# Performance work log

Hardware: AMD Instinct MI355X
Metric: run time of the kernel (lower is better)

## Reference

```python
import jax, jax.numpy as jnp
import numpy as np

B, N1, N2, D = 8, 2048, 2048, 512

def setup_inputs() -> dict:
    key = jax.random.key(0)
    k1, k2, k3, k4 = jax.random.split(key, 4)
    input1 = jax.random.normal(k1, (B, N1, D), dtype=jnp.float32)
    input2 = jax.random.normal(k2, (B, N2, D), dtype=jnp.float32)
    # nn.Linear(D, D): weight [D, D] (out, in), bias [D]
    W_w = jax.random.normal(k3, (D, D), dtype=jnp.float32) * (1.0 / np.sqrt(D))
    W_b = jax.random.normal(k4, (D,), dtype=jnp.float32) * 0.01
    return {"input1": input1, "input2": input2, "W_w": W_w, "W_b": W_b}

def reference(input1, input2, W_w, W_b):
    # q = W(input1): [B, N1, D]
    q = jnp.einsum('bnd,od->bno', input1, W_w) + W_b
    # unscaled scores softmax over last dim (keys N2)
    attn = jax.nn.softmax(jnp.einsum('bnd,bmd->bnm', q, input2), axis=-1)  # [B, N1, N2]
    output1 = jnp.einsum('bnm,bmd->bnd', attn, input2)   # [B, N1, D]
    output2 = jnp.einsum('bnm,bnd->bmd', attn, input1)   # attn^T @ input1 -> [B, N2, D]
    return (output1, output2)
```

## Files before the change

### kernel.cpp

```cpp
#include <hip/hip_runtime.h>


typedef _Float16 f16x8 __attribute__((ext_vector_type(8)));
typedef float floatx4 __attribute__((ext_vector_type(4)));
typedef __attribute__((address_space(1))) const void* gptr_t;
typedef __attribute__((address_space(3))) void* lptr_t;

union F8 { f16x8 v; _Float16 h[8]; unsigned short u[8]; unsigned w[4]; };

__device__ __forceinline__ void gld16(const void* g, void* l) {
    __builtin_amdgcn_global_load_lds((gptr_t)g, (lptr_t)l, 16, 0, 0);
}
__device__ __forceinline__ floatx4 mfma16(f16x8 a, f16x8 b, floatx4 c) {
    return __builtin_amdgcn_mfma_f32_16x16x32_f16(a, b, c, 0, 0, 0);
}

template <int ROWS>
__device__ __forceinline__ void stage64(const _Float16* g, int ldg,
                                        _Float16* lds, int tid) {
#pragma unroll
    for (int c = 0; c < (ROWS * 8) / 256; ++c) {
        const int q = c * 256 + tid;
        const int row = q >> 3;
        const int oct = (q & 7) ^ (row & 7);
        gld16(g + (size_t)row * ldg + oct * 8, lds + q * 8);
    }
}
__device__ __forceinline__ f16x8 ldfrag64(const _Float16* lds, int row, int j) {
    return *(const f16x8*)&lds[row * 64 + ((j ^ (row & 7)) << 3)];
}

template <int ROWS>
__device__ __forceinline__ void stage128(const _Float16* g, int ldg,
                                         _Float16* lds, int tid) {
#pragma unroll
    for (int c = 0; c < (ROWS * 16) / 256; ++c) {
        const int q = c * 256 + tid;
        const int row = q >> 4;
        const int oct = (q & 15) ^ (row & 15);
        gld16(g + (size_t)row * ldg + oct * 8, lds + q * 8);
    }
}
__device__ __forceinline__ f16x8 ldfrag128(const _Float16* lds, int row, int j) {
    return *(const f16x8*)&lds[row * 128 + ((j ^ (row & 15)) << 3)];
}

__global__ __launch_bounds__(256) void k_prep2(
    const float* __restrict__ in1, const float* __restrict__ in2,
    _Float16* __restrict__ x16, _Float16* __restrict__ xt,
    _Float16* __restrict__ k16, _Float16* __restrict__ vt)
{
    const int z = blockIdx.z;
    const int b = z & 7;
    const float* src = (z < 8 ? in1 : in2);
    _Float16* rowo = (z < 8 ? x16 : k16);
    _Float16* colo = (z < 8 ? xt : vt);
    const int d0 = blockIdx.x * 128, n0 = blockIdx.y * 32;
    const float* Sp = src + (size_t)b * 2048 * 512;
    _Float16* Rp = rowo + (size_t)b * 2048 * 512;
    _Float16* Cp = colo + (size_t)b * 512 * 2048;
    const int t = threadIdx.x, i = t & 63, jn = t >> 6;
    const int d = d0 + 2 * i, n = n0 + jn * 8;
    F8 w0, w1;
#pragma unroll
    for (int j = 0; j < 8; j++) {
        float2 g = *(const float2*)(Sp + (size_t)(n + j) * 512 + d);
        w0.h[j] = (_Float16)g.x; w1.h[j] = (_Float16)g.y;
        F8 r; r.h[0] = w0.h[j]; r.h[1] = w1.h[j];
        *(unsigned*)(Rp + (size_t)(n + j) * 512 + d) = r.w[0];
    }
    *(f16x8*)(Cp + (size_t)d * 2048 + n) = w0.v;
    *(f16x8*)(Cp + (size_t)(d + 1) * 2048 + n) = w1.v;
}

__global__ __launch_bounds__(256) void k_cvt(const float* __restrict__ src,
                                             _Float16* __restrict__ dst)
{
    const size_t i = ((size_t)blockIdx.x * 256 + threadIdx.x) * 8;
    float4 a = *(const float4*)(src + i);
    float4 b = *(const float4*)(src + i + 4);
    F8 w;
    w.h[0] = (_Float16)a.x; w.h[1] = (_Float16)a.y;
    w.h[2] = (_Float16)a.z; w.h[3] = (_Float16)a.w;
    w.h[4] = (_Float16)b.x; w.h[5] = (_Float16)b.y;
    w.h[6] = (_Float16)b.z; w.h[7] = (_Float16)b.w;
    *(f16x8*)(dst + i) = w.v;
}

__global__ __launch_bounds__(256, 4) void k_qgemm16(
    const _Float16* __restrict__ A, const _Float16* __restrict__ W,
    const float* __restrict__ bias, _Float16* __restrict__ q)
{
    __shared__ __align__(16) _Float16 As[128 * 64], Bs[128 * 64];
    const int tid = threadIdx.x;
    const int lane = tid & 63, wave = tid >> 6;
    const int wM = (wave >> 1) * 64, wN = (wave & 1) * 64;
    const int lrow = lane & 15, kq = lane >> 4;
    const int bi = blockIdx.x;
    const int r0 = (bi >> 2) * 128, c0 = (bi & 3) * 128;

    floatx4 acc[4][4];
#pragma unroll
    for (int i = 0; i < 4; i++)
#pragma unroll
        for (int j = 0; j < 4; j++) acc[i][j] = (floatx4){0.f, 0.f, 0.f, 0.f};

    for (int k0 = 0; k0 < 512; k0 += 64) {
        stage64<128>(A + (size_t)r0 * 512 + k0, 512, As, tid);
        stage64<128>(W + (size_t)c0 * 512 + k0, 512, Bs, tid);
        __syncthreads();
#pragma unroll
        for (int ks = 0; ks < 2; ks++) {
            f16x8 a[4], b[4];
#pragma unroll
            for (int i = 0; i < 4; i++) {
                a[i] = ldfrag64(As, wM + i * 16 + lrow, ks * 4 + kq);
                b[i] = ldfrag64(Bs, wN + i * 16 + lrow, ks * 4 + kq);
            }
#pragma unroll
            for (int mi = 0; mi < 4; mi++)
#pragma unroll
                for (int ni = 0; ni < 4; ni++)
                    acc[mi][ni] = mfma16(a[mi], b[ni], acc[mi][ni]);
        }
        __syncthreads();
    }
#pragma unroll
    for (int ni = 0; ni < 4; ni++) {
        const int col = c0 + wN + ni * 16 + lrow;
        const float bv = bias[col];
#pragma unroll
        for (int mi = 0; mi < 4; mi++) {
            const int row = r0 + wM + mi * 16 + kq * 4;
#pragma unroll
            for (int r = 0; r < 4; r++)
                q[(size_t)(row + r) * 512 + col] = (_Float16)(acc[mi][ni][r] + bv);
        }
    }
}

__global__ __launch_bounds__(256, 4) void k_scores16(
    const _Float16* __restrict__ q, const _Float16* __restrict__ k,
    _Float16* __restrict__ S)
{
    __shared__ __align__(16) _Float16 As[128 * 64], Bs[128 * 64];
    const int tid = threadIdx.x;
    const int lane = tid & 63, wave = tid >> 6;
    const int wM = (wave >> 1) * 64, wN = (wave & 1) * 64;
    const int lrow = lane & 15, kq = lane >> 4;
    const int bi = blockIdx.x;
    const int bz = bi & 7, t = bi >> 3;
    const int c0 = (t & 15) * 128, r0 = (t >> 4) * 128;
    const _Float16* qp = q + (size_t)bz * 2048 * 512;
    const _Float16* kp = k + (size_t)bz * 2048 * 512;
    _Float16* Sp = S + (size_t)bz * 2048 * 2048;

    floatx4 acc[4][4];
#pragma unroll
    for (int i = 0; i < 4; i++)
#pragma unroll
        for (int j = 0; j < 4; j++) acc[i][j] = (floatx4){0.f, 0.f, 0.f, 0.f};

    for (int k0 = 0; k0 < 512; k0 += 64) {
        stage64<128>(qp + (size_t)r0 * 512 + k0, 512, As, tid);
        stage64<128>(kp + (size_t)c0 * 512 + k0, 512, Bs, tid);
        __syncthreads();
#pragma unroll
        for (int ks = 0; ks < 2; ks++) {
            f16x8 a[4], b[4];
#pragma unroll
            for (int i = 0; i < 4; i++) {
                a[i] = ldfrag64(As, wM + i * 16 + lrow, ks * 4 + kq);
                b[i] = ldfrag64(Bs, wN + i * 16 + lrow, ks * 4 + kq);
            }
#pragma unroll
            for (int mi = 0; mi < 4; mi++)
#pragma unroll
                for (int ni = 0; ni < 4; ni++)
                    acc[mi][ni] = mfma16(a[mi], b[ni], acc[mi][ni]);
        }
        __syncthreads();
    }
#pragma unroll
    for (int mi = 0; mi < 4; mi++)
#pragma unroll
        for (int ni = 0; ni < 4; ni++) {
            const int row = r0 + wM + mi * 16 + kq * 4;
            const int col = c0 + wN + ni * 16 + lrow;
            _Float16* dst = Sp + (size_t)row * 2048 + col;
#pragma unroll
            for (int r = 0; r < 4; r++) dst[(size_t)r * 2048] = (_Float16)acc[mi][ni][r];
        }
}

__global__ __launch_bounds__(256) void k_softmax(const _Float16* __restrict__ S,
                                                 _Float16* __restrict__ P)
{
    const int row = blockIdx.x;
    const _Float16* s = S + (size_t)row * 2048;
    _Float16* p = P + (size_t)row * 2048;
    const int tid = threadIdx.x;
    const int lane = tid & 63, wave = tid >> 6;

    F8 raw;
    raw.v = *(const f16x8*)(s + tid * 8);
    float v[8];
#pragma unroll
    for (int i = 0; i < 8; i++) v[i] = (float)raw.h[i];
    float m = fmaxf(fmaxf(fmaxf(v[0], v[1]), fmaxf(v[2], v[3])),
                    fmaxf(fmaxf(v[4], v[5]), fmaxf(v[6], v[7])));
#pragma unroll
    for (int off = 32; off >= 1; off >>= 1) m = fmaxf(m, __shfl_down(m, off));
    __shared__ float rb[4];
    if (lane == 0) rb[wave] = m;
    __syncthreads();
    m = fmaxf(fmaxf(rb[0], rb[1]), fmaxf(rb[2], rb[3]));

    float e[8];
#pragma unroll
    for (int i = 0; i < 8; i++) e[i] = __expf(v[i] - m);
    float sum = ((e[0] + e[1]) + (e[2] + e[3])) + ((e[4] + e[5]) + (e[6] + e[7]));
#pragma unroll
    for (int off = 32; off >= 1; off >>= 1) sum += __shfl_down(sum, off);
    __syncthreads();
    if (lane == 0) rb[wave] = sum;
    __syncthreads();
    const float inv = 1.0f / (((rb[0] + rb[1]) + (rb[2] + rb[3])));

    F8 w;
#pragma unroll
    for (int i = 0; i < 8; i++) w.h[i] = (_Float16)(e[i] * inv);
    *(f16x8*)(p + tid * 8) = w.v;
}

#define ASTR 136
__global__ __launch_bounds__(256, 3) void k_out12(
    const _Float16* __restrict__ P, const _Float16* __restrict__ Vt,
    const _Float16* __restrict__ Xt, float* __restrict__ O1,
    float* __restrict__ O2)
{
    __shared__ __align__(16) _Float16 As[64 * ASTR];
    __shared__ __align__(16) _Float16 Bs[128 * 128];
    const int tid = threadIdx.x;
    const int lane = tid & 63, wave = tid >> 6;
    const int wM = (wave >> 1) * 32, wN = (wave & 1) * 64;
    const int lrow = lane & 15, kq = lane >> 4;
    const bool isO2 = blockIdx.x >= 1024;
    const int bi = blockIdx.x & 1023;
    const int bz = bi & 7, t = bi >> 3;
    const int c0 = (t & 3) * 128, r0 = (t >> 2) * 64;
    const _Float16* Pp = P + (size_t)bz * 2048 * 2048;
    const _Float16* Bp = (isO2 ? Xt : Vt) + (size_t)bz * 512 * 2048;
    float* Op = (isO2 ? O2 : O1) + (size_t)bz * 2048 * 512;

    floatx4 acc[2][4];
#pragma unroll
    for (int i = 0; i < 2; i++)
#pragma unroll
        for (int j = 0; j < 4; j++) acc[i][j] = (floatx4){0.f, 0.f, 0.f, 0.f};

    if (!isO2) {
        for (int k0 = 0; k0 < 2048; k0 += 128) {
            stage128<64>(Pp + (size_t)r0 * 2048 + k0, 2048, As, tid);
            stage128<128>(Bp + (size_t)c0 * 2048 + k0, 2048, Bs, tid);
            __syncthreads();
#pragma unroll
            for (int ks = 0; ks < 4; ks++) {
                f16x8 a[2], b[4];
#pragma unroll
                for (int i = 0; i < 2; i++)
                    a[i] = ldfrag128(As, wM + i * 16 + lrow, ks * 4 + kq);
#pragma unroll
                for (int i = 0; i < 4; i++)
                    b[i] = ldfrag128(Bs, wN + i * 16 + lrow, ks * 4 + kq);
#pragma unroll
                for (int mi = 0; mi < 2; mi++)
#pragma unroll
                    for (int ni = 0; ni < 4; ni++)
                        acc[mi][ni] = mfma16(a[mi], b[ni], acc[mi][ni]);
            }
            __syncthreads();
        }
    } else {
        const int mPair = (tid & 31) * 2;
        const int kOct0 = tid >> 5;
        for (int k0 = 0; k0 < 2048; k0 += 128) {
            stage128<128>(Bp + (size_t)c0 * 2048 + k0, 2048, Bs, tid);
#pragma unroll
            for (int kh = 0; kh < 2; kh++) {
                const int kOct = kOct0 + kh * 8;
                F8 w0, w1;
#pragma unroll
                for (int j = 0; j < 8; j++) {
                    const unsigned g = *(const unsigned*)(
                        Pp + (size_t)(k0 + kOct * 8 + j) * 2048 + r0 + mPair);
                    w0.u[j] = (unsigned short)(g & 0xffffu);
                    w1.u[j] = (unsigned short)(g >> 16);
                }
                *(f16x8*)&As[mPair * ASTR + kOct * 8] = w0.v;
                *(f16x8*)&As[(mPair + 1) * ASTR + kOct * 8] = w1.v;
            }
            __syncthreads();
#pragma unroll
            for (int ks = 0; ks < 4; ks++) {
                f16x8 a[2], b[4];
#pragma unroll
                for (int i = 0; i < 2; i++)
                    a[i] = *(const f16x8*)&As[(wM + i * 16 + lrow) * ASTR +
                                              (ks * 4 + kq) * 8];
#pragma unroll
                for (int i = 0; i < 4; i++)
                    b[i] = ldfrag128(Bs, wN + i * 16 + lrow, ks * 4 + kq);
#pragma unroll
                for (int mi = 0; mi < 2; mi++)
#pragma unroll
                    for (int ni = 0; ni < 4; ni++)
                        acc[mi][ni] = mfma16(a[mi], b[ni], acc[mi][ni]);
            }
            __syncthreads();
        }
    }
#pragma unroll
    for (int mi = 0; mi < 2; mi++)
#pragma unroll
        for (int ni = 0; ni < 4; ni++) {
            const int row = r0 + wM + mi * 16 + kq * 4;
            const int col = c0 + wN + ni * 16 + lrow;
            float* dst = Op + (size_t)row * 512 + col;
#pragma unroll
            for (int r = 0; r < 4; r++) dst[(size_t)r * 512] = acc[mi][ni][r];
        }
}

extern "C" void kernel_launch(void* const* d_in, const int* in_sizes, int n_in,
                              void* d_out, int out_size, void* d_ws, size_t ws_size,
                              hipStream_t stream)
{
    (void)in_sizes; (void)n_in; (void)out_size; (void)ws_size;
    const float* in1 = (const float*)d_in[0];
    const float* in2 = (const float*)d_in[1];
    const float* Ww  = (const float*)d_in[2];
    const float* Wb  = (const float*)d_in[3];
    float* out = (float*)d_out;

    char* ws = (char*)d_ws;
    _Float16* S   = (_Float16*)ws;
    _Float16* P   = (_Float16*)(ws + 67108864ull);
    _Float16* q16 = (_Float16*)(ws + 134217728ull);
    _Float16* x16 = (_Float16*)(ws + 150994944ull);
    _Float16* k16 = (_Float16*)(ws + 167772160ull);
    _Float16* vt  = (_Float16*)(ws + 184549376ull);
    _Float16* xt  = (_Float16*)(ws + 201326592ull);
    _Float16* w16 = (_Float16*)(ws + 218103808ull);

    k_prep2<<<dim3(4, 64, 16), 256, 0, stream>>>(in1, in2, x16, xt, k16, vt);
    k_cvt <<<128, 256, 0, stream>>>(Ww, w16);
    k_qgemm16<<<512, 256, 0, stream>>>(x16, w16, Wb, q16);
    k_scores16<<<2048, 256, 0, stream>>>(q16, k16, S);
    k_softmax<<<16384, 256, 0, stream>>>(S, P);
    k_out12<<<2048, 256, 0, stream>>>(P, vt, xt, out, out + 8388608);
}
```

Before: 307.7 us.

## Double-buffer output GEMMs, split out kernels, wave-per-row softmax, LDS-tiled transpose prep

The combined output kernel is split into separate O1 and O2 kernels. Both now double-buffer their LDS tiles, and O2 prefetches its transposed P loads into registers so global latency overlaps the MFMA work. Softmax now gives each wave one full row, using xor shuffles with no block barriers. The prep kernel transposes through an LDS tile so its global reads and writes are wide and coalesced. The cost is more LDS per block, which lowers occupancy for O2 (launch bound 2), plus an extra kernel launch.

```diff
diff --git a/kernel.cpp b/kernel.cpp
--- a/kernel.cpp
+++ b/kernel.cpp
@@ -2,11 +2,13 @@
 
 
 typedef _Float16 f16x8 __attribute__((ext_vector_type(8)));
+typedef _Float16 f16x4 __attribute__((ext_vector_type(4)));
 typedef float floatx4 __attribute__((ext_vector_type(4)));
 typedef __attribute__((address_space(1))) const void* gptr_t;
 typedef __attribute__((address_space(3))) void* lptr_t;
 
 union F8 { f16x8 v; _Float16 h[8]; unsigned short u[8]; unsigned w[4]; };
+union F4 { f16x4 v; _Float16 h[4]; unsigned u2[2]; };
 
 __device__ __forceinline__ void gld16(const void* g, void* l) {
     __builtin_amdgcn_global_load_lds((gptr_t)g, (lptr_t)l, 16, 0, 0);
@@ -45,32 +47,46 @@
     return *(const f16x8*)&lds[row * 128 + ((j ^ (row & 15)) << 3)];
 }
 
+#define TS 66
 __global__ __launch_bounds__(256) void k_prep2(
     const float* __restrict__ in1, const float* __restrict__ in2,
     _Float16* __restrict__ x16, _Float16* __restrict__ xt,
     _Float16* __restrict__ k16, _Float16* __restrict__ vt)
 {
+    __shared__ __align__(16) _Float16 T[64 * TS];
     const int z = blockIdx.z;
     const int b = z & 7;
     const float* src = (z < 8 ? in1 : in2);
     _Float16* rowo = (z < 8 ? x16 : k16);
     _Float16* colo = (z < 8 ? xt : vt);
-    const int d0 = blockIdx.x * 128, n0 = blockIdx.y * 32;
+    const int d0 = blockIdx.x * 64, n0 = blockIdx.y * 64;
     const float* Sp = src + (size_t)b * 2048 * 512;
     _Float16* Rp = rowo + (size_t)b * 2048 * 512;
     _Float16* Cp = colo + (size_t)b * 512 * 2048;
-    const int t = threadIdx.x, i = t & 63, jn = t >> 6;
-    const int d = d0 + 2 * i, n = n0 + jn * 8;
+    const int t = threadIdx.x;
+
+#pragma unroll
+    for (int c = 0; c < 4; c++) {
+        const int q = c * 256 + t, r = q >> 4, c4 = q & 15;
+        const float4 g = *(const float4*)(Sp + (size_t)(n0 + r) * 512 + d0 + c4 * 4);
+        F4 w;
+        w.h[0] = (_Float16)g.x; w.h[1] = (_Float16)g.y;
+        w.h[2] = (_Float16)g.z; w.h[3] = (_Float16)g.w;
+        *(f16x4*)(Rp + (size_t)(n0 + r) * 512 + d0 + c4 * 4) = w.v;
+        *(unsigned*)&T[r * TS + c4 * 4]     = w.u2[0];
+        *(unsigned*)&T[r * TS + c4 * 4 + 2] = w.u2[1];
+    }
+    __syncthreads();
+    const int c8 = t & 7, drp = (t >> 3) * 2;
     F8 w0, w1;
 #pragma unroll
-    for (int j = 0; j < 8; j++) {
-        float2 g = *(const float2*)(Sp + (size_t)(n + j) * 512 + d);
-        w0.h[j] = (_Float16)g.x; w1.h[j] = (_Float16)g.y;
-        F8 r; r.h[0] = w0.h[j]; r.h[1] = w1.h[j];
-        *(unsigned*)(Rp + (size_t)(n + j) * 512 + d) = r.w[0];
-    }
-    *(f16x8*)(Cp + (size_t)d * 2048 + n) = w0.v;
-    *(f16x8*)(Cp + (size_t)(d + 1) * 2048 + n) = w1.v;
+    for (int i = 0; i < 8; i++) {
+        const unsigned g = *(const unsigned*)&T[(c8 * 8 + i) * TS + drp];
+        w0.u[i] = (unsigned short)(g & 0xffffu);
+        w1.u[i] = (unsigned short)(g >> 16);
+    }
+    *(f16x8*)(Cp + (size_t)(d0 + drp) * 2048 + n0 + c8 * 8) = w0.v;
+    *(f16x8*)(Cp + (size_t)(d0 + drp + 1) * 2048 + n0 + c8 * 8) = w1.v;
 }
 
 __global__ __launch_bounds__(256) void k_cvt(const float* __restrict__ src,
@@ -196,62 +212,56 @@
 __global__ __launch_bounds__(256) void k_softmax(const _Float16* __restrict__ S,
                                                  _Float16* __restrict__ P)
 {
-    const int row = blockIdx.x;
+    const int wave = threadIdx.x >> 6, lane = threadIdx.x & 63;
+    const int row = blockIdx.x * 4 + wave;
     const _Float16* s = S + (size_t)row * 2048;
     _Float16* p = P + (size_t)row * 2048;
-    const int tid = threadIdx.x;
-    const int lane = tid & 63, wave = tid >> 6;
-
-    F8 raw;
-    raw.v = *(const f16x8*)(s + tid * 8);
-    float v[8];
-#pragma unroll
-    for (int i = 0; i < 8; i++) v[i] = (float)raw.h[i];
-    float m = fmaxf(fmaxf(fmaxf(v[0], v[1]), fmaxf(v[2], v[3])),
-                    fmaxf(fmaxf(v[4], v[5]), fmaxf(v[6], v[7])));
-#pragma unroll
-    for (int off = 32; off >= 1; off >>= 1) m = fmaxf(m, __shfl_down(m, off));
-    __shared__ float rb[4];
-    if (lane == 0) rb[wave] = m;
-    __syncthreads();
-    m = fmaxf(fmaxf(rb[0], rb[1]), fmaxf(rb[2], rb[3]));
-
-    float e[8];
-#pragma unroll
-    for (int i = 0; i < 8; i++) e[i] = __expf(v[i] - m);
-    float sum = ((e[0] + e[1]) + (e[2] + e[3])) + ((e[4] + e[5]) + (e[6] + e[7]));
-#pragma unroll
-    for (int off = 32; off >= 1; off >>= 1) sum += __shfl_down(sum, off);
-    __syncthreads();
-    if (lane == 0) rb[wave] = sum;
-    __syncthreads();
-    const float inv = 1.0f / (((rb[0] + rb[1]) + (rb[2] + rb[3])));
-
-    F8 w;
-#pragma unroll
-    for (int i = 0; i < 8; i++) w.h[i] = (_Float16)(e[i] * inv);
-    *(f16x8*)(p + tid * 8) = w.v;
-}
-
-#define ASTR 136
-__global__ __launch_bounds__(256, 3) void k_out12(
+
+    F8 raw[4];
+    float v[32];
+#pragma unroll
+    for (int c = 0; c < 4; c++) {
+        raw[c].v = *(const f16x8*)(s + c * 512 + lane * 8);
+#pragma unroll
+        for (int i = 0; i < 8; i++) v[c * 8 + i] = (float)raw[c].h[i];
+    }
+    float m = v[0];
+#pragma unroll
+    for (int i = 1; i < 32; i++) m = fmaxf(m, v[i]);
+#pragma unroll
+    for (int off = 32; off >= 1; off >>= 1) m = fmaxf(m, __shfl_xor(m, off));
+
+    float sum = 0.f;
+#pragma unroll
+    for (int i = 0; i < 32; i++) { v[i] = __expf(v[i] - m); sum += v[i]; }
+#pragma unroll
+    for (int off = 32; off >= 1; off >>= 1) sum += __shfl_xor(sum, off);
+    const float inv = 1.0f / sum;
+
+#pragma unroll
+    for (int c = 0; c < 4; c++) {
+        F8 w;
+#pragma unroll
+        for (int i = 0; i < 8; i++) w.h[i] = (_Float16)(v[c * 8 + i] * inv);
+        *(f16x8*)(p + c * 512 + lane * 8) = w.v;
+    }
+}
+
+__global__ __launch_bounds__(256, 3) void k_out1(
     const _Float16* __restrict__ P, const _Float16* __restrict__ Vt,
-    const _Float16* __restrict__ Xt, float* __restrict__ O1,
-    float* __restrict__ O2)
-{
-    __shared__ __align__(16) _Float16 As[64 * ASTR];
-    __shared__ __align__(16) _Float16 Bs[128 * 128];
+    float* __restrict__ O1)
+{
+    __shared__ __align__(16) _Float16 As[2][64 * 64], Bs[2][128 * 64];
     const int tid = threadIdx.x;
     const int lane = tid & 63, wave = tid >> 6;
     const int wM = (wave >> 1) * 32, wN = (wave & 1) * 64;
     const int lrow = lane & 15, kq = lane >> 4;
-    const bool isO2 = blockIdx.x >= 1024;
-    const int bi = blockIdx.x & 1023;
+    const int bi = blockIdx.x;
     const int bz = bi & 7, t = bi >> 3;
     const int c0 = (t & 3) * 128, r0 = (t >> 2) * 64;
     const _Float16* Pp = P + (size_t)bz * 2048 * 2048;
-    const _Float16* Bp = (isO2 ? Xt : Vt) + (size_t)bz * 512 * 2048;
-    float* Op = (isO2 ? O2 : O1) + (size_t)bz * 2048 * 512;
+    const _Float16* Bp = Vt + (size_t)bz * 512 * 2048;
+    float* Op = O1 + (size_t)bz * 2048 * 512;
 
     floatx4 acc[2][4];
 #pragma unroll
@@ -259,66 +269,125 @@
 #pragma unroll
         for (int j = 0; j < 4; j++) acc[i][j] = (floatx4){0.f, 0.f, 0.f, 0.f};
 
-    if (!isO2) {
-        for (int k0 = 0; k0 < 2048; k0 += 128) {
-            stage128<64>(Pp + (size_t)r0 * 2048 + k0, 2048, As, tid);
-            stage128<128>(Bp + (size_t)c0 * 2048 + k0, 2048, Bs, tid);
-            __syncthreads();
-#pragma unroll
-            for (int ks = 0; ks < 4; ks++) {
-                f16x8 a[2], b[4];
-#pragma unroll
-                for (int i = 0; i < 2; i++)
-                    a[i] = ldfrag128(As, wM + i * 16 + lrow, ks * 4 + kq);
-#pragma unroll
-                for (int i = 0; i < 4; i++)
-                    b[i] = ldfrag128(Bs, wN + i * 16 + lrow, ks * 4 + kq);
-#pragma unroll
-                for (int mi = 0; mi < 2; mi++)
-#pragma unroll
-                    for (int ni = 0; ni < 4; ni++)
-                        acc[mi][ni] = mfma16(a[mi], b[ni], acc[mi][ni]);
+    stage64<64>(Pp + (size_t)r0 * 2048, 2048, As[0], tid);
+    stage64<128>(Bp + (size_t)c0 * 2048, 2048, Bs[0], tid);
+    __syncthreads();
+    int cur = 0;
+    for (int k0 = 0; k0 < 2048; k0 += 64) {
+        if (k0 < 2048 - 64) {
+            stage64<64>(Pp + (size_t)r0 * 2048 + k0 + 64, 2048, As[cur ^ 1], tid);
+            stage64<128>(Bp + (size_t)c0 * 2048 + k0 + 64, 2048, Bs[cur ^ 1], tid);
+        }
+        const _Float16* Ac = As[cur];
+        const _Float16* Bc = Bs[cur];
+#pragma unroll
+        for (int ks = 0; ks < 2; ks++) {
+            f16x8 a[2], b[4];
+#pragma unroll
+            for (int i = 0; i < 2; i++)
+                a[i] = ldfrag64(Ac, wM + i * 16 + lrow, ks * 4 + kq);
+#pragma unroll
+            for (int i = 0; i < 4; i++)
+                b[i] = ldfrag64(Bc, wN + i * 16 + lrow, ks * 4 + kq);
+#pragma unroll
+            for (int mi = 0; mi < 2; mi++)
+#pragma unroll
+                for (int ni = 0; ni < 4; ni++)
+                    acc[mi][ni] = mfma16(a[mi], b[ni], acc[mi][ni]);
+        }
+        __syncthreads();
+        cur ^= 1;
+    }
+#pragma unroll
+    for (int mi = 0; mi < 2; mi++)
+#pragma unroll
+        for (int ni = 0; ni < 4; ni++) {
+            const int row = r0 + wM + mi * 16 + kq * 4;
+            const int col = c0 + wN + ni * 16 + lrow;
+            float* dst = Op + (size_t)row * 512 + col;
+#pragma unroll
+            for (int r = 0; r < 4; r++) dst[(size_t)r * 512] = acc[mi][ni][r];
+        }
+}
+
+__device__ __forceinline__ void loadtr(const _Float16* Pp, int r0, int mPair,
+                                       int kOct0, int k0, unsigned (&u)[16]) {
+#pragma unroll
+    for (int kh = 0; kh < 2; kh++)
+#pragma unroll
+        for (int j = 0; j < 8; j++)
+            u[kh * 8 + j] = *(const unsigned*)(
+                Pp + (size_t)(k0 + (kOct0 + kh * 8) * 8 + j) * 2048 + r0 + mPair);
+}
+
+__global__ __launch_bounds__(256, 2) void k_out2(
+    const _Float16* __restrict__ P, const _Float16* __restrict__ Xt,
+    float* __restrict__ O2)
+{
+    __shared__ __align__(16) _Float16 As[64 * 128];
+    __shared__ __align__(16) _Float16 Bs[2][128 * 128];
+    const int tid = threadIdx.x;
+    const int lane = tid & 63, wave = tid >> 6;
+    const int wM = (wave >> 1) * 32, wN = (wave & 1) * 64;
+    const int lrow = lane & 15, kq = lane >> 4;
+    const int bi = blockIdx.x;
+    const int bz = bi & 7, t = bi >> 3;
+    const int c0 = (t & 3) * 128, r0 = (t >> 2) * 64;
+    const _Float16* Pp = P + (size_t)bz * 2048 * 2048;
+    const _Float16* Bp = Xt + (size_t)bz * 512 * 2048;
+    float* Op = O2 + (size_t)bz * 2048 * 512;
+
+    const int mPair = (tid & 31) * 2;
+    const int kOct0 = tid >> 5;
+
+    floatx4 acc[2][4];
+#pragma unroll
+    for (int i = 0; i < 2; i++)
+#pragma unroll
+        for (int j = 0; j < 4; j++) acc[i][j] = (floatx4){0.f, 0.f, 0.f, 0.f};
+
+    unsigned u[16];
+    loadtr(Pp, r0, mPair, kOct0, 0, u);
+    stage128<128>(Bp + (size_t)c0 * 2048, 2048, Bs[0], tid);
+    int cur = 0;
+    for (int k0 = 0; k0 < 2048; k0 += 128) {
+#pragma unroll
+        for (int kh = 0; kh < 2; kh++) {
+            const int kOct = kOct0 + kh * 8;
+            F8 w0, w1;
+#pragma unroll
+            for (int j = 0; j < 8; j++) {
+                const unsigned g = u[kh * 8 + j];
+                w0.u[j] = (unsigned short)(g & 0xffffu);
+                w1.u[j] = (unsigned short)(g >> 16);
             }
-            __syncthreads();
-        }
-    } else {
-        const int mPair = (tid & 31) * 2;
-        const int kOct0 = tid >> 5;
-        for (int k0 = 0; k0 < 2048; k0 += 128) {
-            stage128<128>(Bp + (size_t)c0 * 2048 + k0, 2048, Bs, tid);
-#pragma unroll
-            for (int kh = 0; kh < 2; kh++) {
-                const int kOct = kOct0 + kh * 8;
-                F8 w0, w1;
-#pragma unroll
-                for (int j = 0; j < 8; j++) {
-                    const unsigned g = *(const unsigned*)(
-                        Pp + (size_t)(k0 + kOct * 8 + j) * 2048 + r0 + mPair);
-                    w0.u[j] = (unsigned short)(g & 0xffffu);
-                    w1.u[j] = (unsigned short)(g >> 16);
-                }
-                *(f16x8*)&As[mPair * ASTR + kOct * 8] = w0.v;
-                *(f16x8*)&As[(mPair + 1) * ASTR + kOct * 8] = w1.v;
-            }
-            __syncthreads();
-#pragma unroll
-            for (int ks = 0; ks < 4; ks++) {
-                f16x8 a[2], b[4];
-#pragma unroll
-                for (int i = 0; i < 2; i++)
-                    a[i] = *(const f16x8*)&As[(wM + i * 16 + lrow) * ASTR +
-                                              (ks * 4 + kq) * 8];
-#pragma unroll
-                for (int i = 0; i < 4; i++)
-                    b[i] = ldfrag128(Bs, wN + i * 16 + lrow, ks * 4 + kq);
-#pragma unroll
-                for (int mi = 0; mi < 2; mi++)
-#pragma unroll
-                    for (int ni = 0; ni < 4; ni++)
-                        acc[mi][ni] = mfma16(a[mi], b[ni], acc[mi][ni]);
-            }
-            __syncthreads();
-        }
+            *(f16x8*)&As[mPair * 128 + ((kOct ^ (mPair & 15)) << 3)] = w0.v;
+            *(f16x8*)&As[(mPair + 1) * 128 + ((kOct ^ ((mPair + 1) & 15)) << 3)] = w1.v;
+        }
+        __syncthreads();
+        if (k0 < 2048 - 128) {
+            loadtr(Pp, r0, mPair, kOct0, k0 + 128, u);
+            stage128<128>(Bp + (size_t)c0 * 2048 + k0 + 128, 2048,
+                          Bs[cur ^ 1], tid);
+        }
+        const _Float16* Bc = Bs[cur];
+#pragma unroll
+        for (int ks = 0; ks < 4; ks++) {
+            f16x8 a[2], b[4];
+#pragma unroll
+            for (int i = 0; i < 2; i++)
+                a[i] = ldfrag128(As, wM + i * 16 + lrow, ks * 4 + kq);
+#pragma unroll
+            for (int i = 0; i < 4; i++)
+                b[i] = ldfrag128(Bc, wN + i * 16 + lrow, ks * 4 + kq);
+#pragma unroll
+            for (int mi = 0; mi < 2; mi++)
+#pragma unroll
+                for (int ni = 0; ni < 4; ni++)
+                    acc[mi][ni] = mfma16(a[mi], b[ni], acc[mi][ni]);
+        }
+        __syncthreads();
+        cur ^= 1;
     }
 #pragma unroll
     for (int mi = 0; mi < 2; mi++)
@@ -353,10 +422,11 @@
     _Float16* xt  = (_Float16*)(ws + 201326592ull);
     _Float16* w16 = (_Float16*)(ws + 218103808ull);
 
-    k_prep2<<<dim3(4, 64, 16), 256, 0, stream>>>(in1, in2, x16, xt, k16, vt);
+    k_prep2<<<dim3(8, 32, 16), 256, 0, stream>>>(in1, in2, x16, xt, k16, vt);
     k_cvt <<<128, 256, 0, stream>>>(Ww, w16);
     k_qgemm16<<<512, 256, 0, stream>>>(x16, w16, Wb, q16);
     k_scores16<<<2048, 256, 0, stream>>>(q16, k16, S);
-    k_softmax<<<16384, 256, 0, stream>>>(S, P);
-    k_out12<<<2048, 256, 0, stream>>>(P, vt, xt, out, out + 8388608);
-}
+    k_softmax<<<4096, 256, 0, stream>>>(S, P);
+    k_out2<<<1024, 256, 0, stream>>>(P, xt, out + 8388608);
+    k_out1<<<1024, 256, 0, stream>>>(P, vt, out);
+}
```

Result: slower. 321.0 us (+4.3%).
